# Optimization experiments

Hardware: AMD Instinct MI355X
Metric: run time of the kernel (lower is better)

## Reference

```python
import jax, jax.numpy as jnp
import numpy as np

# module hyper-parameters (from init_kwargs)
IN_H, IN_W = 64, 44
OUT_H, OUT_W = 48, 22
DT_OFF, DX_OFF, DY_OFF = 0.5, 0.5, 0.5
SIGMA_OFF, DELTA_OFF = 1.0, 1.0
EPS = 1e-8
K_PO = 2  # ProgressiveOffset k


def _progressive_offset(v, k=K_PO):
    # torch: x += detach(x) shifted right by i with zero fill, scaled 1/k, for i=1..k
    vd = jax.lax.stop_gradient(v)
    out = v
    T = v.shape[1]
    for i in range(1, k + 1):
        out = out + jnp.pad(vd, ((0, 0), (i, 0)))[:, :T] * (1.0 / k)
    return out


def setup_inputs() -> dict:
    key = jax.random.key(0)
    ks = jax.random.split(key, 9)
    N, C, T = 16, 64, 30
    return {
        "x": jax.random.normal(ks[0], (N, C, T, IN_H, IN_W), jnp.float32),
        "dx": jax.random.normal(ks[1], (N, T), jnp.float32),
        "dy": jax.random.normal(ks[2], (N, T), jnp.float32),
        "log_sigma2": jax.random.normal(ks[3], (N, T), jnp.float32),
        "log_delta": jax.random.normal(ks[4], (N, T), jnp.float32),
        "log_gamma": jax.random.normal(ks[5], (N, T), jnp.float32),
        "dt": jax.random.normal(ks[6], (N,), jnp.float32),
        "log_delta_t": jax.random.normal(ks[7], (N,), jnp.float32),
        "log_gamma_t": jax.random.normal(ks[8], (N,), jnp.float32),
    }


def reference(x, dx, dy, log_sigma2, log_delta, log_gamma, dt, log_delta_t, log_gamma_t):
    N, C, T, H, W = x.shape
    NT = N * T
    a_w = OUT_W
    a_h = int(round(OUT_W / IN_W * IN_H))  # attended spatial height (32)

    anchor_t = T * DT_OFF
    anchor_x = W * DX_OFF
    anchor_y = H * DY_OFF

    # --- localization params ---
    dxv = jnp.tanh(_progressive_offset(dx).reshape(NT, 1)) * (IN_W / 2.0) + anchor_x
    dyv = jnp.tanh(_progressive_offset(dy).reshape(NT, 1)) * (IN_H / 2.0) + anchor_y
    sigma2 = jnp.exp(log_sigma2).reshape(NT, 1) * SIGMA_OFF
    delta = jnp.exp(log_delta).reshape(NT, 1) * DELTA_OFF
    gamma = jax.nn.sigmoid(log_gamma).reshape(NT)
    dtv = jnp.tanh(dt) * (T / 2.0) + anchor_t           # (N,)
    delta_t = jnp.exp(log_delta_t) * DELTA_OFF          # (N,)
    gamma_t = jax.nn.sigmoid(log_gamma_t)               # (N,)

    # --- Gaussian spatial filter banks ---
    gx = jnp.arange(a_w, dtype=x.dtype)
    gy = jnp.arange(a_h, dtype=x.dtype)
    mu_x = dxv + (gx[None, :] - a_w / 2.0) * delta      # (NT, a_w)
    mu_y = dyv + (gy[None, :] - a_h / 2.0) * delta      # (NT, a_h)
    a = jnp.arange(W, dtype=x.dtype)[None, None, :]
    b = jnp.arange(H, dtype=x.dtype)[None, None, :]
    s2 = sigma2[:, :, None]                              # (NT,1,1)
    Fx = jnp.exp(-((a - mu_x[:, :, None]) ** 2) / (2.0 * s2))  # (NT, a_w, W)
    Fy = jnp.exp(-((b - mu_y[:, :, None]) ** 2) / (2.0 * s2))  # (NT, a_h, H)
    Fx = Fx / jnp.maximum(jnp.sum(Fx, axis=2, keepdims=True), EPS)
    Fy = Fy / jnp.maximum(jnp.sum(Fy, axis=2, keepdims=True), EPS)

    # --- spatial glimpse: Fy @ x @ Fx^T, batched over (N*T, C) ---
    xf = jnp.transpose(x, (0, 2, 1, 3, 4)).reshape(NT, C, H, W)
    glimpse = jnp.einsum('nih,nchw,njw->ncij', Fy, xf, Fx)  # (NT, C, a_h, a_w)
    glimpse = glimpse * gamma[:, None, None, None]

    # --- temporal transform (grid_sample, align_corners=False, zero padding) ---
    gt = jnp.arange(T, dtype=x.dtype)
    mu_t = dtv[:, None] + (gt[None, :] - T / 2.0) * delta_t[:, None]  # (N, T)
    mu_t = mu_t / (T - 1) * 2.0 - 1.0
    # y-axis sample coords in input index space
    iy = ((mu_t + 1.0) * T - 1.0) / 2.0
    iy0 = jnp.floor(iy)
    w1 = iy - iy0
    w0 = 1.0 - w1
    i0 = iy0.astype(jnp.int32)
    i1 = i0 + 1
    v0 = ((i0 >= 0) & (i0 < T)).astype(x.dtype)
    v1 = ((i1 >= 0) & (i1 < T)).astype(x.dtype)
    g = glimpse.reshape(N, T, C * a_h * a_w)             # (N, T, Chw)
    g0 = jnp.take_along_axis(g, jnp.clip(i0, 0, T - 1)[:, :, None], axis=1)
    g1 = jnp.take_along_axis(g, jnp.clip(i1, 0, T - 1)[:, :, None], axis=1)
    # x-grid coord is fixed at -1 with width-1 input -> factor 0.5 (half in zero pad)
    out_t = 0.5 * ((w0 * v0)[:, :, None] * g0 + (w1 * v1)[:, :, None] * g1)

    out = out_t.reshape(N, T, C, a_h, a_w).transpose(0, 2, 1, 3, 4)  # (N,C,T,a_h,a_w)
    out = out * gamma_t[:, None, None, None, None]

    pad_t = (OUT_H - a_h) // 2
    pad_b = OUT_H - pad_t - a_h
    out = jnp.pad(out, ((0, 0), (0, 0), (0, 0), (pad_t, pad_b), (0, 0)))
    return out
```

## Files before the change

kernel.cpp:

```cpp
#include <hip/hip_runtime.h>
#include <math.h>


#define EPS_ 1e-8f

__global__ __launch_bounds__(256) void gst_kernel(
    const float* __restrict__ x,
    const float* __restrict__ dx,  const float* __restrict__ dy,
    const float* __restrict__ ls2, const float* __restrict__ ld,
    const float* __restrict__ lg,
    const float* __restrict__ dtp, const float* __restrict__ ldt,
    const float* __restrict__ lgt,
    float* __restrict__ out)
{
    __shared__ float FyT[64][36];
    __shared__ float FxT[44][24];
    __shared__ float t2s[8][64][24];

    const int tid = threadIdx.x;
    int b = blockIdx.x;
    const int cg = b & 7; b >>= 3;
    const int tq = b % 30;
    const int n  = b / 30;

    const float dtv     = tanhf(dtp[n]) * 15.f + 15.f;
    const float delta_t = expf(ldt[n]);
    const float gamma_t = 1.f / (1.f + expf(-lgt[n]));
    float mu_t = dtv + ((float)tq - 15.f) * delta_t;
    mu_t = mu_t / 29.f * 2.f - 1.f;
    const float iy  = ((mu_t + 1.f) * 30.f - 1.f) * 0.5f;
    const float iy0 = floorf(iy);
    const float w1  = iy - iy0;
    const int   i0  = (int)iy0;
    const int   i1  = i0 + 1;
    const float W0 = (i0 >= 0 && i0 < 30) ? 0.5f * gamma_t * (1.f - w1) : 0.f;
    const float W1 = (i1 >= 0 && i1 < 30) ? 0.5f * gamma_t * w1 : 0.f;
    const int t0 = min(max(i0, 0), 29);
    const int t1 = min(max(i1, 0), 29);

    const int c_loc = tid >> 5;
    const int hp    = tid & 31;
    const int jt    = tid & 3;
    const int it    = (tid >> 2) & 7;
    const int j0    = 6 * jt;
    const int i0r   = 4 * it;

    float acc2[4][6];
#pragma unroll
    for (int r = 0; r < 4; ++r)
#pragma unroll
        for (int s2 = 0; s2 < 6; ++s2) acc2[r][s2] = 0.f;

#pragma unroll 1
    for (int s = 0; s < 2; ++s) {
        const float Ws = s ? W1 : W0;
        const int   ts = s ? t1 : t0;
        if (Ws == 0.f) continue;

        __syncthreads();

        {
            const int nt = n * 30 + ts;
            const float sigma2 = expf(ls2[nt]);
            const float inv2s2 = 0.5f / sigma2;
            const float delta  = expf(ld[nt]);
            const float gamma  = 1.f / (1.f + expf(-lg[nt]));
            const float A      = Ws * gamma;
            if (tid < 32) {
                float pod = dy[nt] + 0.5f * (ts >= 1 ? dy[nt - 1] : 0.f)
                                   + 0.5f * (ts >= 2 ? dy[nt - 2] : 0.f);
                const float muy = tanhf(pod) * 32.f + 32.f;
                const float mu  = muy + ((float)tid - 16.f) * delta;
                float sum = 0.f;
                for (int h = 0; h < 64; ++h) {
                    float d = (float)h - mu; sum += expf(-d * d * inv2s2);
                }
                const float sc = A / fmaxf(sum, EPS_);
                for (int h = 0; h < 64; ++h) {
                    float d = (float)h - mu;
                    FyT[h][tid] = expf(-d * d * inv2s2) * sc;
                }
            } else if (tid < 54) {
                const int j = tid - 32;
                float pod = dx[nt] + 0.5f * (ts >= 1 ? dx[nt - 1] : 0.f)
                                   + 0.5f * (ts >= 2 ? dx[nt - 2] : 0.f);
                const float mux = tanhf(pod) * 22.f + 22.f;
                const float mu  = mux + ((float)j - 11.f) * delta;
                float sum = 0.f;
                for (int w = 0; w < 44; ++w) {
                    float d = (float)w - mu; sum += expf(-d * d * inv2s2);
                }
                const float sc = 1.f / fmaxf(sum, EPS_);
                for (int w = 0; w < 44; ++w) {
                    float d = (float)w - mu;
                    FxT[w][j] = expf(-d * d * inv2s2) * sc;
                }
            }
        }
        __syncthreads();

        {
            float a0[22], a1[22];
#pragma unroll
            for (int j = 0; j < 22; ++j) { a0[j] = 0.f; a1[j] = 0.f; }

            const size_t xoff =
                ((((size_t)n * 64 + (size_t)(cg * 8 + c_loc)) * 30 + (size_t)ts) * 64
                 + (size_t)(2 * hp)) * 44;
            const float4* xr0 = reinterpret_cast<const float4*>(x + xoff);
            const float4* xr1 = reinterpret_cast<const float4*>(x + xoff + 44);

#pragma unroll 2
            for (int wi = 0; wi < 11; ++wi) {
                const float4 xa = xr0[wi];
                const float4 xb = xr1[wi];
                const float xav[4] = { xa.x, xa.y, xa.z, xa.w };
                const float xbv[4] = { xb.x, xb.y, xb.z, xb.w };
#pragma unroll
                for (int k = 0; k < 4; ++k) {
                    const float4* fxr =
                        reinterpret_cast<const float4*>(&FxT[4 * wi + k][0]);
                    const float4 f0 = fxr[0], f1 = fxr[1], f2 = fxr[2],
                                 f3 = fxr[3], f4 = fxr[4];
                    const float2 f5 =
                        *reinterpret_cast<const float2*>(&FxT[4 * wi + k][20]);
                    const float fv[22] = { f0.x, f0.y, f0.z, f0.w,
                                           f1.x, f1.y, f1.z, f1.w,
                                           f2.x, f2.y, f2.z, f2.w,
                                           f3.x, f3.y, f3.z, f3.w,
                                           f4.x, f4.y, f4.z, f4.w,
                                           f5.x, f5.y };
                    const float va = xav[k], vb = xbv[k];
#pragma unroll
                    for (int j = 0; j < 22; ++j) {
                        a0[j] += va * fv[j];
                        a1[j] += vb * fv[j];
                    }
                }
            }
            float4* d0 = reinterpret_cast<float4*>(&t2s[c_loc][2 * hp][0]);
            float4* d1 = reinterpret_cast<float4*>(&t2s[c_loc][2 * hp + 1][0]);
            d0[0] = make_float4(a0[0],  a0[1],  a0[2],  a0[3]);
            d0[1] = make_float4(a0[4],  a0[5],  a0[6],  a0[7]);
            d0[2] = make_float4(a0[8],  a0[9],  a0[10], a0[11]);
            d0[3] = make_float4(a0[12], a0[13], a0[14], a0[15]);
            d0[4] = make_float4(a0[16], a0[17], a0[18], a0[19]);
            d0[5] = make_float4(a0[20], a0[21], 0.f, 0.f);
            d1[0] = make_float4(a1[0],  a1[1],  a1[2],  a1[3]);
            d1[1] = make_float4(a1[4],  a1[5],  a1[6],  a1[7]);
            d1[2] = make_float4(a1[8],  a1[9],  a1[10], a1[11]);
            d1[3] = make_float4(a1[12], a1[13], a1[14], a1[15]);
            d1[4] = make_float4(a1[16], a1[17], a1[18], a1[19]);
            d1[5] = make_float4(a1[20], a1[21], 0.f, 0.f);
        }
        __syncthreads();

        {
#pragma unroll 2
            for (int h4 = 0; h4 < 16; ++h4) {
#pragma unroll
                for (int k = 0; k < 4; ++k) {
                    const int h = 4 * h4 + k;
                    const float4 fy =
                        *reinterpret_cast<const float4*>(&FyT[h][i0r]);
                    const float2* tp =
                        reinterpret_cast<const float2*>(&t2s[c_loc][h][j0]);
                    const float2 q0 = tp[0], q1 = tp[1], q2 = tp[2];
                    const float fyv[4] = { fy.x, fy.y, fy.z, fy.w };
                    const float tv[6]  = { q0.x, q0.y, q1.x, q1.y, q2.x, q2.y };
#pragma unroll
                    for (int r = 0; r < 4; ++r)
#pragma unroll
                        for (int s2 = 0; s2 < 6; ++s2)
                            acc2[r][s2] += fyv[r] * tv[s2];
                }
            }
        }
    }

    const size_t ob =
        (((size_t)n * 64 + (size_t)(cg * 8)) * 30 + (size_t)tq) * 1056;

    for (int idx = tid; idx < 8 * 16 * 22; idx += 256) {
        const int c   = idx / 352;
        const int rem = idx % 352;
        const int r   = rem / 22;
        const int j   = rem % 22;
        const int ip  = (r < 8) ? r : (r + 32);
        out[ob + (size_t)c * 31680 + (size_t)(ip * 22 + j)] = 0.f;
    }

#pragma unroll
    for (int r = 0; r < 4; ++r) {
#pragma unroll
        for (int s2 = 0; s2 < 6; ++s2) {
            const int j = j0 + s2;
            if (j < 22) {
                out[ob + (size_t)c_loc * 31680
                       + (size_t)((8 + i0r + r) * 22 + j)] = acc2[r][s2];
            }
        }
    }
}

extern "C" void kernel_launch(void* const* d_in, const int* in_sizes, int n_in,
                              void* d_out, int out_size, void* d_ws, size_t ws_size,
                              hipStream_t stream) {
    const float* x   = (const float*)d_in[0];
    const float* dx  = (const float*)d_in[1];
    const float* dy  = (const float*)d_in[2];
    const float* ls2 = (const float*)d_in[3];
    const float* ld  = (const float*)d_in[4];
    const float* lg  = (const float*)d_in[5];
    const float* dtp = (const float*)d_in[6];
    const float* ldt = (const float*)d_in[7];
    const float* lgt = (const float*)d_in[8];
    float* out = (float*)d_out;

    dim3 grid(16 * 30 * 8), block(256);
    hipLaunchKernelGGL(gst_kernel, grid, block, 0, stream,
                       x, dx, dy, ls2, ld, lg, dtp, ldt, lgt, out);
}
```

Before: 685.2 us.

## Split into per-frame glimpse pass and temporal interpolation pass via workspace

Computes the spatial Gaussian glimpse once per (n,t,c) into a workspace buffer, then a second kernel blends two glimpse frames for the temporal grid-sample and writes the padded output. This removes the redundant re-reading of x and the repeated filter-bank and matmul work for frames used by two output time steps. Filter-bank construction is also parallelized across more threads with shuffle reductions. The cost is an extra intermediate buffer round trip and a second launch, and the fused kernel remains as a fallback when the workspace is too small.

```diff
diff --git a/kernel.cpp b/kernel.cpp
--- a/kernel.cpp
+++ b/kernel.cpp
@@ -1,23 +1,168 @@
 #include <hip/hip_runtime.h>
 #include <math.h>
 
-
 #define EPS_ 1e-8f
 
-__global__ __launch_bounds__(256) void gst_kernel(
+__global__ __launch_bounds__(256) void gst_phase1(
     const float* __restrict__ x,
     const float* __restrict__ dx,  const float* __restrict__ dy,
     const float* __restrict__ ls2, const float* __restrict__ ld,
     const float* __restrict__ lg,
+    float* __restrict__ g)
+{
+    __shared__ float FyT[64][32];
+    __shared__ float FxT[44][24];
+    __shared__ float t2s[4][64][22];
+
+    const int tid = threadIdx.x;
+    int b = blockIdx.x;
+    const int cg = b & 15; b >>= 4;
+    const int nt = b;
+    const int ts = nt % 30;
+    const int n  = nt / 30;
+
+    const float sigma2 = expf(ls2[nt]);
+    const float inv2s2 = 0.5f / sigma2;
+    const float delta  = expf(ld[nt]);
+    const float gamma  = 1.f / (1.f + expf(-lg[nt]));
+
+    {
+        const float pod = dy[nt] + 0.5f * (ts >= 1 ? dy[nt - 1] : 0.f)
+                                 + 0.5f * (ts >= 2 ? dy[nt - 2] : 0.f);
+        const float muy = tanhf(pod) * 32.f + 32.f;
+        const int i  = tid >> 3;
+        const int hg = tid & 7;
+        const float mu = muy + ((float)i - 16.f) * delta;
+        float e[8];
+        float sum = 0.f;
+#pragma unroll
+        for (int k = 0; k < 8; ++k) {
+            const float d = (float)(8 * hg + k) - mu;
+            e[k] = expf(-d * d * inv2s2);
+            sum += e[k];
+        }
+        sum += __shfl_xor(sum, 1);
+        sum += __shfl_xor(sum, 2);
+        sum += __shfl_xor(sum, 4);
+        const float sc = gamma / fmaxf(sum, EPS_);
+#pragma unroll
+        for (int k = 0; k < 8; ++k) FyT[8 * hg + k][i] = e[k] * sc;
+    }
+    if (tid < 176) {
+        const float pod = dx[nt] + 0.5f * (ts >= 1 ? dx[nt - 1] : 0.f)
+                                 + 0.5f * (ts >= 2 ? dx[nt - 2] : 0.f);
+        const float mux = tanhf(pod) * 22.f + 22.f;
+        const int j  = tid >> 3;
+        const int wg = tid & 7;
+        const float mu = mux + ((float)j - 11.f) * delta;
+        float e[6];
+        float sum = 0.f;
+#pragma unroll
+        for (int k = 0; k < 6; ++k) {
+            const int w = 6 * wg + k;
+            const float d = (float)w - mu;
+            const float v = (w < 44) ? expf(-d * d * inv2s2) : 0.f;
+            e[k] = v; sum += v;
+        }
+        sum += __shfl_xor(sum, 1);
+        sum += __shfl_xor(sum, 2);
+        sum += __shfl_xor(sum, 4);
+        const float sc = 1.f / fmaxf(sum, EPS_);
+#pragma unroll
+        for (int k = 0; k < 6; ++k) {
+            const int w = 6 * wg + k;
+            if (w < 44) FxT[w][j] = e[k] * sc;
+        }
+    }
+    __syncthreads();
+
+    const int c_loc = tid >> 6;
+    const int c     = cg * 4 + c_loc;
+
+    {
+        const int h = tid & 63;
+        float a[22];
+#pragma unroll
+        for (int j = 0; j < 22; ++j) a[j] = 0.f;
+
+        const size_t xoff =
+            ((((size_t)n * 64 + (size_t)c) * 30 + (size_t)ts) * 64 + (size_t)h) * 44;
+        const float4* xr = reinterpret_cast<const float4*>(x + xoff);
+
+#pragma unroll 2
+        for (int wi = 0; wi < 11; ++wi) {
+            const float4 xa = xr[wi];
+            const float xv[4] = { xa.x, xa.y, xa.z, xa.w };
+#pragma unroll
+            for (int k = 0; k < 4; ++k) {
+                const int w = 4 * wi + k;
+                const float4* fx = reinterpret_cast<const float4*>(&FxT[w][0]);
+                const float4 f0 = fx[0], f1 = fx[1], f2 = fx[2], f3 = fx[3], f4 = fx[4];
+                const float2 f5 = *reinterpret_cast<const float2*>(&FxT[w][20]);
+                const float fv[22] = { f0.x, f0.y, f0.z, f0.w,
+                                       f1.x, f1.y, f1.z, f1.w,
+                                       f2.x, f2.y, f2.z, f2.w,
+                                       f3.x, f3.y, f3.z, f3.w,
+                                       f4.x, f4.y, f4.z, f4.w,
+                                       f5.x, f5.y };
+                const float va = xv[k];
+#pragma unroll
+                for (int j = 0; j < 22; ++j) a[j] += va * fv[j];
+            }
+        }
+        float2* dst = reinterpret_cast<float2*>(&t2s[c_loc][h][0]);
+#pragma unroll
+        for (int q = 0; q < 11; ++q) dst[q] = make_float2(a[2 * q], a[2 * q + 1]);
+    }
+    __syncthreads();
+
+    {
+        const int lt = tid & 63;
+        const int jt = lt & 3;
+        const int it = lt >> 2;
+        const int j0 = 6 * jt;
+        const int i0 = 2 * it;
+
+        float acc[2][6];
+#pragma unroll
+        for (int r = 0; r < 2; ++r)
+#pragma unroll
+            for (int s = 0; s < 6; ++s) acc[r][s] = 0.f;
+
+#pragma unroll 4
+        for (int h = 0; h < 64; ++h) {
+            const float2 fy = *reinterpret_cast<const float2*>(&FyT[h][i0]);
+            const float2* tp = reinterpret_cast<const float2*>(&t2s[c_loc][h][j0]);
+            const float2 q0 = tp[0], q1 = tp[1], q2 = tp[2];
+            const float fyv[2] = { fy.x, fy.y };
+            const float tv[6]  = { q0.x, q0.y, q1.x, q1.y, q2.x, q2.y };
+#pragma unroll
+            for (int r = 0; r < 2; ++r)
+#pragma unroll
+                for (int s = 0; s < 6; ++s) acc[r][s] += fyv[r] * tv[s];
+        }
+
+        const size_t gbase = ((size_t)nt * 64 + (size_t)c) * 704;
+#pragma unroll
+        for (int r = 0; r < 2; ++r) {
+#pragma unroll
+            for (int s2 = 0; s2 < 3; ++s2) {
+                const int j = j0 + 2 * s2;
+                if (j < 22) {
+                    *reinterpret_cast<float2*>(g + gbase + (size_t)((i0 + r) * 22 + j)) =
+                        make_float2(acc[r][2 * s2], acc[r][2 * s2 + 1]);
+                }
+            }
+        }
+    }
+}
+
+__global__ __launch_bounds__(256) void gst_phase2(
+    const float* __restrict__ g,
     const float* __restrict__ dtp, const float* __restrict__ ldt,
     const float* __restrict__ lgt,
     float* __restrict__ out)
 {
-    __shared__ float FyT[64][36];
-    __shared__ float FxT[44][24];
-    __shared__ float t2s[8][64][24];
-
-    const int tid = threadIdx.x;
     int b = blockIdx.x;
     const int cg = b & 7; b >>= 3;
     const int tq = b % 30;
@@ -38,6 +183,62 @@
     const int t0 = min(max(i0, 0), 29);
     const int t1 = min(max(i1, 0), 29);
 
+    const size_t ob  = (((size_t)n * 64 + (size_t)cg * 8) * 30 + (size_t)tq) * 1056;
+    const size_t g0b = ((size_t)(n * 30 + t0) * 64 + (size_t)cg * 8) * 704;
+    const size_t g1b = ((size_t)(n * 30 + t1) * 64 + (size_t)cg * 8) * 704;
+
+    for (int idx = threadIdx.x; idx < 4224; idx += 256) {
+        const int c   = idx / 528;
+        const int e2  = idx - c * 528;
+        const int pos = e2 * 2;
+        const int ip  = pos / 22;
+        const int j   = pos - ip * 22;
+        float2 v = make_float2(0.f, 0.f);
+        if (ip >= 8 && ip < 40) {
+            const size_t go = (size_t)c * 704 + (size_t)((ip - 8) * 22 + j);
+            const float2 a  = *reinterpret_cast<const float2*>(g + g0b + go);
+            const float2 bb = *reinterpret_cast<const float2*>(g + g1b + go);
+            v.x = W0 * a.x + W1 * bb.x;
+            v.y = W0 * a.y + W1 * bb.y;
+        }
+        *reinterpret_cast<float2*>(out + ob + (size_t)c * 31680 + pos) = v;
+    }
+}
+
+__global__ __launch_bounds__(256) void gst_fused(
+    const float* __restrict__ x,
+    const float* __restrict__ dx,  const float* __restrict__ dy,
+    const float* __restrict__ ls2, const float* __restrict__ ld,
+    const float* __restrict__ lg,
+    const float* __restrict__ dtp, const float* __restrict__ ldt,
+    const float* __restrict__ lgt,
+    float* __restrict__ out)
+{
+    __shared__ float FyT[64][36];
+    __shared__ float FxT[44][24];
+    __shared__ float t2s[8][64][24];
+
+    const int tid = threadIdx.x;
+    int b = blockIdx.x;
+    const int cg = b & 7; b >>= 3;
+    const int tq = b % 30;
+    const int n  = b / 30;
+
+    const float dtv     = tanhf(dtp[n]) * 15.f + 15.f;
+    const float delta_t = expf(ldt[n]);
+    const float gamma_t = 1.f / (1.f + expf(-lgt[n]));
+    float mu_t = dtv + ((float)tq - 15.f) * delta_t;
+    mu_t = mu_t / 29.f * 2.f - 1.f;
+    const float iy  = ((mu_t + 1.f) * 30.f - 1.f) * 0.5f;
+    const float iy0 = floorf(iy);
+    const float w1  = iy - iy0;
+    const int   i0  = (int)iy0;
+    const int   i1  = i0 + 1;
+    const float W0 = (i0 >= 0 && i0 < 30) ? 0.5f * gamma_t * (1.f - w1) : 0.f;
+    const float W1 = (i1 >= 0 && i1 < 30) ? 0.5f * gamma_t * w1 : 0.f;
+    const int t0 = min(max(i0, 0), 29);
+    const int t1 = min(max(i1, 0), 29);
+
     const int c_loc = tid >> 5;
     const int hp    = tid & 31;
     const int jt    = tid & 3;
@@ -56,9 +257,7 @@
         const float Ws = s ? W1 : W0;
         const int   ts = s ? t1 : t0;
         if (Ws == 0.f) continue;
-
         __syncthreads();
-
         {
             const int nt = n * 30 + ts;
             const float sigma2 = expf(ls2[nt]);
@@ -98,18 +297,15 @@
             }
         }
         __syncthreads();
-
         {
             float a0[22], a1[22];
 #pragma unroll
             for (int j = 0; j < 22; ++j) { a0[j] = 0.f; a1[j] = 0.f; }
-
             const size_t xoff =
                 ((((size_t)n * 64 + (size_t)(cg * 8 + c_loc)) * 30 + (size_t)ts) * 64
                  + (size_t)(2 * hp)) * 44;
             const float4* xr0 = reinterpret_cast<const float4*>(x + xoff);
             const float4* xr1 = reinterpret_cast<const float4*>(x + xoff + 44);
-
 #pragma unroll 2
             for (int wi = 0; wi < 11; ++wi) {
                 const float4 xa = xr0[wi];
@@ -118,69 +314,54 @@
                 const float xbv[4] = { xb.x, xb.y, xb.z, xb.w };
 #pragma unroll
                 for (int k = 0; k < 4; ++k) {
-                    const float4* fxr =
-                        reinterpret_cast<const float4*>(&FxT[4 * wi + k][0]);
-                    const float4 f0 = fxr[0], f1 = fxr[1], f2 = fxr[2],
-                                 f3 = fxr[3], f4 = fxr[4];
-                    const float2 f5 =
-                        *reinterpret_cast<const float2*>(&FxT[4 * wi + k][20]);
-                    const float fv[22] = { f0.x, f0.y, f0.z, f0.w,
-                                           f1.x, f1.y, f1.z, f1.w,
-                                           f2.x, f2.y, f2.z, f2.w,
-                                           f3.x, f3.y, f3.z, f3.w,
-                                           f4.x, f4.y, f4.z, f4.w,
-                                           f5.x, f5.y };
+                    const float4* fxr = reinterpret_cast<const float4*>(&FxT[4 * wi + k][0]);
+                    const float4 f0 = fxr[0], f1 = fxr[1], f2 = fxr[2], f3 = fxr[3], f4 = fxr[4];
+                    const float2 f5 = *reinterpret_cast<const float2*>(&FxT[4 * wi + k][20]);
+                    const float fv[22] = { f0.x, f0.y, f0.z, f0.w, f1.x, f1.y, f1.z, f1.w,
+                                           f2.x, f2.y, f2.z, f2.w, f3.x, f3.y, f3.z, f3.w,
+                                           f4.x, f4.y, f4.z, f4.w, f5.x, f5.y };
                     const float va = xav[k], vb = xbv[k];
 #pragma unroll
-                    for (int j = 0; j < 22; ++j) {
-                        a0[j] += va * fv[j];
-                        a1[j] += vb * fv[j];
-                    }
+                    for (int j = 0; j < 22; ++j) { a0[j] += va * fv[j]; a1[j] += vb * fv[j]; }
                 }
             }
             float4* d0 = reinterpret_cast<float4*>(&t2s[c_loc][2 * hp][0]);
             float4* d1 = reinterpret_cast<float4*>(&t2s[c_loc][2 * hp + 1][0]);
-            d0[0] = make_float4(a0[0],  a0[1],  a0[2],  a0[3]);
-            d0[1] = make_float4(a0[4],  a0[5],  a0[6],  a0[7]);
-            d0[2] = make_float4(a0[8],  a0[9],  a0[10], a0[11]);
+            d0[0] = make_float4(a0[0], a0[1], a0[2], a0[3]);
+            d0[1] = make_float4(a0[4], a0[5], a0[6], a0[7]);
+            d0[2] = make_float4(a0[8], a0[9], a0[10], a0[11]);
             d0[3] = make_float4(a0[12], a0[13], a0[14], a0[15]);
             d0[4] = make_float4(a0[16], a0[17], a0[18], a0[19]);
             d0[5] = make_float4(a0[20], a0[21], 0.f, 0.f);
-            d1[0] = make_float4(a1[0],  a1[1],  a1[2],  a1[3]);
-            d1[1] = make_float4(a1[4],  a1[5],  a1[6],  a1[7]);
-            d1[2] = make_float4(a1[8],  a1[9],  a1[10], a1[11]);
+            d1[0] = make_float4(a1[0], a1[1], a1[2], a1[3]);
+            d1[1] = make_float4(a1[4], a1[5], a1[6], a1[7]);
+            d1[2] = make_float4(a1[8], a1[9], a1[10], a1[11]);
             d1[3] = make_float4(a1[12], a1[13], a1[14], a1[15]);
             d1[4] = make_float4(a1[16], a1[17], a1[18], a1[19]);
             d1[5] = make_float4(a1[20], a1[21], 0.f, 0.f);
         }
         __syncthreads();
-
         {
 #pragma unroll 2
             for (int h4 = 0; h4 < 16; ++h4) {
 #pragma unroll
                 for (int k = 0; k < 4; ++k) {
                     const int h = 4 * h4 + k;
-                    const float4 fy =
-                        *reinterpret_cast<const float4*>(&FyT[h][i0r]);
-                    const float2* tp =
-                        reinterpret_cast<const float2*>(&t2s[c_loc][h][j0]);
+                    const float4 fy = *reinterpret_cast<const float4*>(&FyT[h][i0r]);
+                    const float2* tp = reinterpret_cast<const float2*>(&t2s[c_loc][h][j0]);
                     const float2 q0 = tp[0], q1 = tp[1], q2 = tp[2];
                     const float fyv[4] = { fy.x, fy.y, fy.z, fy.w };
                     const float tv[6]  = { q0.x, q0.y, q1.x, q1.y, q2.x, q2.y };
 #pragma unroll
                     for (int r = 0; r < 4; ++r)
 #pragma unroll
-                        for (int s2 = 0; s2 < 6; ++s2)
-                            acc2[r][s2] += fyv[r] * tv[s2];
-                }
-            }
-        }
-    }
-
-    const size_t ob =
-        (((size_t)n * 64 + (size_t)(cg * 8)) * 30 + (size_t)tq) * 1056;
-
+                        for (int s2 = 0; s2 < 6; ++s2) acc2[r][s2] += fyv[r] * tv[s2];
+                }
+            }
+        }
+    }
+
+    const size_t ob = (((size_t)n * 64 + (size_t)(cg * 8)) * 30 + (size_t)tq) * 1056;
     for (int idx = tid; idx < 8 * 16 * 22; idx += 256) {
         const int c   = idx / 352;
         const int rem = idx % 352;
@@ -189,15 +370,13 @@
         const int ip  = (r < 8) ? r : (r + 32);
         out[ob + (size_t)c * 31680 + (size_t)(ip * 22 + j)] = 0.f;
     }
-
 #pragma unroll
     for (int r = 0; r < 4; ++r) {
 #pragma unroll
         for (int s2 = 0; s2 < 6; ++s2) {
             const int j = j0 + s2;
             if (j < 22) {
-                out[ob + (size_t)c_loc * 31680
-                       + (size_t)((8 + i0r + r) * 22 + j)] = acc2[r][s2];
+                out[ob + (size_t)c_loc * 31680 + (size_t)((8 + i0r + r) * 22 + j)] = acc2[r][s2];
             }
         }
     }
@@ -217,7 +396,16 @@
     const float* lgt = (const float*)d_in[8];
     float* out = (float*)d_out;
 
-    dim3 grid(16 * 30 * 8), block(256);
-    hipLaunchKernelGGL(gst_kernel, grid, block, 0, stream,
-                       x, dx, dy, ls2, ld, lg, dtp, ldt, lgt, out);
+    const size_t g_bytes = (size_t)480 * 64 * 704 * sizeof(float);
+
+    if (ws_size >= g_bytes) {
+        float* g = (float*)d_ws;
+        hipLaunchKernelGGL(gst_phase1, dim3(480 * 16), dim3(256), 0, stream,
+                           x, dx, dy, ls2, ld, lg, g);
+        hipLaunchKernelGGL(gst_phase2, dim3(16 * 30 * 8), dim3(256), 0, stream,
+                           g, dtp, ldt, lgt, out);
+    } else {
+        hipLaunchKernelGGL(gst_fused, dim3(16 * 30 * 8), dim3(256), 0, stream,
+                           x, dx, dy, ls2, ld, lg, dtp, ldt, lgt, out);
+    }
 }
```

Result: no change. 692.9 us (+1.1%).
